# Optimization experiments

Measured on AMD Instinct MI355X. Metric: run time of the kernel, lower is better.

Reference implementation:

```python
import jax, jax.numpy as jnp
import numpy as np
import math

H = 16          # n_head
N_EMBD = 1024
EPS = 1e-5      # torch LayerNorm default


def setup_inputs() -> dict:
    key = jax.random.key(0)
    ks = jax.random.split(key, 6)
    B, T, C = 2, 2048, 1024
    x = jax.random.normal(ks[0], (B, T, C), dtype=jnp.float32)
    s = 0.02  # GPT-2 style init scale keeps softmax logits sane
    Wq = jax.random.normal(ks[1], (C, N_EMBD), dtype=jnp.float32) * s
    Wk = jax.random.normal(ks[2], (C, N_EMBD), dtype=jnp.float32) * s
    Wv = jax.random.normal(ks[3], (C, N_EMBD), dtype=jnp.float32) * s
    Wo = jax.random.normal(ks[4], (N_EMBD, C), dtype=jnp.float32) * s
    return {
        "x": x,
        "Wq": Wq, "bq": jnp.zeros((N_EMBD,), jnp.float32),
        "Wk": Wk, "bk": jnp.zeros((N_EMBD,), jnp.float32),
        "Wv": Wv, "bv": jnp.zeros((N_EMBD,), jnp.float32),
        "Wo": Wo, "bo": jnp.zeros((C,), jnp.float32),
        "gamma": jnp.ones((C,), jnp.float32),
        "beta": jnp.zeros((C,), jnp.float32),
    }


def reference(x, Wq, bq, Wk, bk, Wv, bv, Wo, bo, gamma, beta):
    B, T, _ = x.shape
    Dh = N_EMBD // H
    # projections -> (B, H, T, Dh)
    def split_heads(y):
        return y.reshape(B, T, H, Dh).transpose(0, 2, 1, 3)
    q = split_heads(x @ Wq + bq)
    k = split_heads(x @ Wk + bk)
    v = split_heads(x @ Wv + bv)
    # naive causal attention: explicit (B,H,T,T) scores
    att = jnp.einsum("bhtd,bhsd->bhts", q, k) * (1.0 / math.sqrt(Dh))
    causal = jnp.tril(jnp.ones((T, T), dtype=bool))
    att = jnp.where(causal[None, None], att, -jnp.inf)
    att = jax.nn.softmax(att, axis=-1)
    o = jnp.einsum("bhts,bhsd->bhtd", att, v)
    o = o.transpose(0, 2, 1, 3).reshape(B, T, N_EMBD)
    y = o @ Wo + bo
    # LayerNorm (dropout is identity at p=0 / eval)
    mu = jnp.mean(y, axis=-1, keepdims=True)
    var = jnp.var(y, axis=-1, keepdims=True)
    return (y - mu) * jax.lax.rsqrt(var + EPS) * gamma + beta
```

## Files before the change

kernel.cpp:

```cpp
#include <hip/hip_runtime.h>
#include <stdint.h>
#include <stddef.h>

typedef __attribute__((ext_vector_type(8))) short short8;
typedef __attribute__((ext_vector_type(4))) float f32x4;
typedef __attribute__((ext_vector_type(16))) float f32x16;
typedef __attribute__((ext_vector_type(4))) unsigned short us4;
typedef __attribute__((ext_vector_type(4))) unsigned u32x4;

#define DEVI static __device__ __forceinline__

DEVI unsigned short f2bf(float f) {
  unsigned u = __builtin_bit_cast(unsigned, f);
  u += 0x7FFFu + ((u >> 16) & 1u);
  return (unsigned short)(u >> 16);
}

DEVI f32x4 mfma16(short8 a, short8 b, f32x4 c) {
  return __builtin_amdgcn_mfma_f32_16x16x32_bf16(a, b, c, 0, 0, 0);
}

DEVI f32x16 mfma32(short8 a, short8 b, f32x16 c) {
  return __builtin_amdgcn_mfma_f32_32x32x16_bf16(a, b, c, 0, 0, 0);
}

DEVI unsigned cvtpk(float lo, float hi) {
  unsigned r;
  asm("v_cvt_pk_bf16_f32 %0, %1, %2" : "=v"(r) : "v"(lo), "v"(hi));
  return r;
}

DEVI void plswap(unsigned& a, unsigned& b) {
  asm("v_permlane32_swap_b32 %0, %1" : "+v"(a), "+v"(b));
}

DEVI float ex2(float x) {
  float r;
  asm("v_exp_f32 %0, %1" : "=v"(r) : "v"(x));
  return r;
}

DEVI float mx3(float a, float b, float c) {
  float r;
  asm("v_max3_f32 %0, %1, %2, %3" : "=v"(r) : "v"(a), "v"(b), "v"(c));
  return r;
}

DEVI f32x16 zero16() {
  f32x16 z;
#pragma unroll
  for (int i = 0; i < 16; ++i) z[i] = 0.f;
  return z;
}

DEVI void glds16(const void* g, void* l) {
  __builtin_amdgcn_global_load_lds(
      (const __attribute__((address_space(1))) void*)g,
      (__attribute__((address_space(3))) void*)l, 16, 0, 0);
}

__global__ __launch_bounds__(256) void k_cvt_x(const float* __restrict__ x,
                                               unsigned short* __restrict__ xb) {
  size_t i = ((size_t)blockIdx.x * 256 + threadIdx.x) * 8;
  f32x4 a = *(const f32x4*)(x + i);
  f32x4 b = *(const f32x4*)(x + i + 4);
  short8 v;
#pragma unroll
  for (int j = 0; j < 4; ++j) {
    v[j] = (short)f2bf(a[j]);
    v[4 + j] = (short)f2bf(b[j]);
  }
  *(short8*)(xb + i) = v;
}

__global__ __launch_bounds__(256) void k_twT4(const float* __restrict__ W0,
                                              const float* __restrict__ W1,
                                              const float* __restrict__ W2,
                                              const float* __restrict__ W3,
                                              unsigned short* __restrict__ WT) {
  __shared__ float tile[64][65];
  const int z = blockIdx.z;
  const float* W = (z == 0) ? W0 : (z == 1) ? W1 : (z == 2) ? W2 : W3;
  unsigned short* out = WT + (size_t)z * 1024 * 1024;
  const int n0 = blockIdx.x * 64, k0 = blockIdx.y * 64;
  const int t = threadIdx.x, rr = t >> 4, cc = (t & 15) * 4;
#pragma unroll
  for (int i = 0; i < 4; ++i) {
    int row = i * 16 + rr;
    f32x4 v = *(const f32x4*)(W + (size_t)(k0 + row) * 1024 + n0 + cc);
#pragma unroll
    for (int j = 0; j < 4; ++j) tile[row][cc + j] = v[j];
  }
  __syncthreads();
#pragma unroll
  for (int i = 0; i < 4; ++i) {
    int nrow = i * 16 + rr;
    us4 u;
#pragma unroll
    for (int j = 0; j < 4; ++j) u[j] = f2bf(tile[cc + j][nrow]);
    *(us4*)(out + (size_t)(n0 + nrow) * 1024 + k0 + cc) = u;
  }
}

template <bool SWAP>
DEVI void gemm_core2(const unsigned short* __restrict__ A,
                     const unsigned short* __restrict__ Bt,
                     int mt, int nt, char* lds, f32x4 (&acc)[4][4]) {
  const int t = threadIdx.x;
  const int l = t & 63, c = l & 15, g = l >> 4;
  const int w = t >> 6, wr = w >> 1, wc = w & 1;
  const int srow = t >> 3;
  const int sxor = (((t & 7) ^ (srow & 7))) * 8;
  const unsigned short* Ab = A + (size_t)(mt * 128 + srow) * 1024 + sxor;
  const unsigned short* Bb = Bt + (size_t)(nt * 128 + srow) * 1024 + sxor;
  const int key = (c & 7);

  auto STAGE = [&](int kt, int buf) {
    char* lb = lds + buf * 32768;
#pragma unroll
    for (int i = 0; i < 4; ++i) {
      glds16(Ab + (size_t)i * 32 * 1024 + kt * 64, lb + i * 4096 + t * 16);
      glds16(Bb + (size_t)i * 32 * 1024 + kt * 64, lb + 16384 + i * 4096 + t * 16);
    }
  };

  STAGE(0, 0);
  asm volatile("s_waitcnt vmcnt(0)" ::: "memory");
  __builtin_amdgcn_s_barrier();
  asm volatile("" ::: "memory");
  for (int kt = 0; kt < 16; ++kt) {
    const int cur = kt & 1;
    if (kt < 15) STAGE(kt + 1, cur ^ 1);
    const char* lb = lds + cur * 32768;
#pragma unroll
    for (int ks = 0; ks < 2; ++ks) {
      short8 af[4], bfr[4];
#pragma unroll
      for (int m = 0; m < 4; ++m)
        af[m] = *(const short8*)(lb + (wr * 64 + m * 16 + c) * 128 +
                                 ((ks * 4 + g) ^ key) * 16);
#pragma unroll
      for (int n = 0; n < 4; ++n)
        bfr[n] = *(const short8*)(lb + 16384 + (wc * 64 + n * 16 + c) * 128 +
                                  ((ks * 4 + g) ^ key) * 16);
#pragma unroll
      for (int m = 0; m < 4; ++m)
#pragma unroll
        for (int n = 0; n < 4; ++n)
          acc[m][n] = SWAP ? mfma16(bfr[n], af[m], acc[m][n])
                           : mfma16(af[m], bfr[n], acc[m][n]);
    }
    asm volatile("s_waitcnt vmcnt(0)" ::: "memory");
    __builtin_amdgcn_s_barrier();
    asm volatile("" ::: "memory");
  }
}

__global__ __launch_bounds__(256) void k_gemm_qkv(
    const unsigned short* __restrict__ A,
    const unsigned short* __restrict__ Wf,
    const float* __restrict__ b0, const float* __restrict__ b1, const float* __restrict__ b2,
    unsigned short* __restrict__ O0, unsigned short* __restrict__ O1,
    unsigned short* __restrict__ O2) {
  __shared__ char lds[65536];
  const int mt = blockIdx.x, ntz = blockIdx.y;
  const int z = ntz >> 3, ntl = ntz & 7;
  const float* bias = (z == 0) ? b0 : (z == 1) ? b1 : b2;
  unsigned short* out = (z == 0) ? O0 : (z == 1) ? O1 : O2;
  f32x4 acc[4][4];
#pragma unroll
  for (int m = 0; m < 4; ++m)
#pragma unroll
    for (int n = 0; n < 4; ++n) acc[m][n] = (f32x4){0.f, 0.f, 0.f, 0.f};
  const int t = threadIdx.x, l = t & 63, c = l & 15, g = l >> 4;
  const int w = t >> 6, wr = w >> 1, wc = w & 1;
  if (z < 2) {
    gemm_core2<true>(A, Wf, mt, ntz, lds, acc);
    const float sc = (z == 0) ? 0.18033688011f : 1.0f;
#pragma unroll
    for (int n = 0; n < 4; ++n) {
      int colb = ntl * 128 + wc * 64 + n * 16 + 4 * g;
      f32x4 bv4 = *(const f32x4*)(bias + colb);
      int h = colb >> 6, d = colb & 63;
#pragma unroll
      for (int m = 0; m < 4; ++m) {
        int rowg = mt * 128 + wr * 64 + m * 16 + c;
        int b = rowg >> 11, tt = rowg & 2047;
        us4 u;
#pragma unroll
        for (int r = 0; r < 4; ++r) u[r] = f2bf((acc[m][n][r] + bv4[r]) * sc);
        *(us4*)(out + ((size_t)(b * 16 + h) * 2048 + tt) * 64 + d) = u;
      }
    }
  } else {
    gemm_core2<false>(A, Wf, mt, ntz, lds, acc);
#pragma unroll
    for (int n = 0; n < 4; ++n) {
      int colg = ntl * 128 + wc * 64 + n * 16 + c;
      float bvv = bias[colg];
      int h = colg >> 6, d = colg & 63;
#pragma unroll
      for (int m = 0; m < 4; ++m) {
        int rowg = mt * 128 + wr * 64 + m * 16 + 4 * g;
        int b = rowg >> 11, tt = rowg & 2047;
        us4 u;
#pragma unroll
        for (int r = 0; r < 4; ++r) u[r] = f2bf(acc[m][n][r] + bvv);
        *(us4*)(out + ((size_t)(b * 16 + h) * 64 + d) * 2048 + tt) = u;
      }
    }
  }
}

__global__ __launch_bounds__(256) void k_gemm_proj(const unsigned short* __restrict__ A,
                                                   const unsigned short* __restrict__ Bt,
                                                   const float* __restrict__ bias,
                                                   float* __restrict__ Y) {
  __shared__ char lds[65536];
  f32x4 acc[4][4];
#pragma unroll
  for (int m = 0; m < 4; ++m)
#pragma unroll
    for (int n = 0; n < 4; ++n) acc[m][n] = (f32x4){0.f, 0.f, 0.f, 0.f};
  const int mt = blockIdx.x, nt = blockIdx.y;
  gemm_core2<true>(A, Bt, mt, nt, lds, acc);
  const int t = threadIdx.x, l = t & 63, c = l & 15, g = l >> 4;
  const int w = t >> 6, wr = w >> 1, wc = w & 1;
#pragma unroll
  for (int n = 0; n < 4; ++n) {
    int colb = nt * 128 + wc * 64 + n * 16 + 4 * g;
    f32x4 bv4 = *(const f32x4*)(bias + colb);
#pragma unroll
    for (int m = 0; m < 4; ++m) {
      int rowg = mt * 128 + wr * 64 + m * 16 + c;
      f32x4 o;
#pragma unroll
      for (int r = 0; r < 4; ++r) o[r] = acc[m][n][r] + bv4[r];
      *(f32x4*)(Y + (size_t)rowg * 1024 + colb) = o;
    }
  }
}

__global__ __launch_bounds__(128) void k_attn4(const unsigned short* __restrict__ Q,
                                               const unsigned short* __restrict__ K,
                                               const unsigned short* __restrict__ VT,
                                               unsigned short* __restrict__ O) {
  __shared__ char lds[32768];
  const int bid = blockIdx.x;
  const int half = bid >> 9, j = bid & 511;
  const int qt = half ? (j >> 5) : (31 - (j >> 5));
  const int bh = j & 31;
  const int t = threadIdx.x;
  const int w = t >> 6, l = t & 63;
  const int lq = l & 31, hi = l >> 5;
  const int q0 = qt * 64 + w * 32;
  const size_t kbase = (size_t)bh * 2048 * 64;
  const size_t vbase = (size_t)bh * 64 * 2048;
  const int srow = t >> 3;
  const int sx = ((t & 7) ^ (srow & 7)) * 8;
  const int NT = qt + 1;

  short8 qf[4];
#pragma unroll
  for (int ds = 0; ds < 4; ++ds)
    qf[ds] = *(const short8*)(Q + kbase + (size_t)(q0 + lq) * 64 + 16 * ds + 8 * hi);

  auto STAGE = [&](int kt, int buf) {
    const unsigned short* Kt = K + kbase + (size_t)kt * 4096;
    const unsigned short* Vt = VT + vbase + kt * 64;
    char* lb = lds + buf * 16384;
#pragma unroll
    for (int i = 0; i < 4; ++i) {
      int row = i * 16 + srow;
      glds16(Kt + (size_t)row * 64 + sx, lb + i * 2048 + t * 16);
      glds16(Vt + (size_t)row * 2048 + sx, lb + 8192 + i * 2048 + t * 16);
    }
  };

  f32x16 oacc[2];
  oacc[0] = zero16();
  oacc[1] = zero16();
  float m_s = -1e30f, l_s = 0.f;
  const int rx = lq & 7;

  STAGE(0, 0);
  for (int kt = 0; kt < NT; ++kt) {
    asm volatile("s_waitcnt vmcnt(0)" ::: "memory");
    __builtin_amdgcn_s_barrier();
    asm volatile("" ::: "memory");
    if (kt + 1 < NT) STAGE(kt + 1, (kt + 1) & 1);
    const char* lb = lds + (kt & 1) * 16384;
    const int kv0 = kt * 64;
    short8 kf0[4], kf1[4];
#pragma unroll
    for (int ds = 0; ds < 4; ++ds) {
      int blk = ((ds * 2 + hi) ^ rx) * 16;
      kf0[ds] = *(const short8*)(lb + lq * 128 + blk);
      kf1[ds] = *(const short8*)(lb + (lq + 32) * 128 + blk);
    }
    f32x16 st0 = zero16(), st1 = zero16();
    __builtin_amdgcn_s_setprio(1);
#pragma unroll
    for (int ds = 0; ds < 4; ++ds) {
      st0 = mfma32(kf0[ds], qf[ds], st0);
      st1 = mfma32(kf1[ds], qf[ds], st1);
    }
    __builtin_amdgcn_s_setprio(0);
    short8 vf[2][4];
#pragma unroll
    for (int fd = 0; fd < 2; ++fd) {
      int d = fd * 32 + lq;
#pragma unroll
      for (int s = 0; s < 4; ++s)
        vf[fd][s] = *(const short8*)(lb + 8192 + d * 128 + (((s * 2 + hi) ^ rx) * 16));
    }
    if (kt == NT - 1) {
      const int qg = q0 + lq;
#pragma unroll
      for (int r = 0; r < 16; ++r) {
        int kr = kv0 + (r & 3) + 8 * (r >> 2) + 4 * hi;
        if (kr > qg) st0[r] = -1e30f;
        if (kr + 32 > qg) st1[r] = -1e30f;
      }
    }
    float a8[8];
#pragma unroll
    for (int r = 0; r < 8; ++r)
      a8[r] = fmaxf(mx3(st0[r], st0[r + 8], st1[r]), st1[r + 8]);
    float mxv = mx3(mx3(a8[0], a8[1], a8[2]), mx3(a8[3], a8[4], a8[5]),
                    fmaxf(a8[6], a8[7]));
    mxv = fmaxf(mxv, __shfl_xor(mxv, 32, 64));
    if (!__all(mxv - m_s <= 11.5413f)) {
      float mnew = fmaxf(m_s, mxv);
      float corr = ex2(m_s - mnew);
      m_s = mnew;
      l_s *= corr;
#pragma unroll
      for (int r = 0; r < 16; ++r) {
        oacc[0][r] *= corr;
        oacc[1][r] *= corr;
      }
    }
    unsigned Wp[2][4][2];
    float gs[8];
#pragma unroll
    for (int f = 0; f < 2; ++f)
#pragma unroll
      for (int m4 = 0; m4 < 4; ++m4) {
        float p0 = ex2((f ? st1 : st0)[4 * m4 + 0] - m_s);
        float p1 = ex2((f ? st1 : st0)[4 * m4 + 1] - m_s);
        float p2 = ex2((f ? st1 : st0)[4 * m4 + 2] - m_s);
        float p3 = ex2((f ? st1 : st0)[4 * m4 + 3] - m_s);
        gs[f * 4 + m4] = (p0 + p1) + (p2 + p3);
        Wp[f][m4][0] = cvtpk(p0, p1);
        Wp[f][m4][1] = cvtpk(p2, p3);
      }
    float ps = ((gs[0] + gs[1]) + (gs[2] + gs[3])) + ((gs[4] + gs[5]) + (gs[6] + gs[7]));
    ps += __shfl_xor(ps, 32, 64);
    l_s += ps;
    __builtin_amdgcn_s_setprio(1);
#pragma unroll
    for (int s = 0; s < 4; ++s) {
      const int f = s >> 1, s2 = s & 1;
      unsigned a0 = Wp[f][2 * s2][0], b0 = Wp[f][2 * s2 + 1][0];
      unsigned a1 = Wp[f][2 * s2][1], b1 = Wp[f][2 * s2 + 1][1];
      plswap(a0, b0);
      plswap(a1, b1);
      u32x4 pw = {a0, a1, b0, b1};
      short8 pf = __builtin_bit_cast(short8, pw);
      oacc[0] = mfma32(vf[0][s], pf, oacc[0]);
      oacc[1] = mfma32(vf[1][s], pf, oacc[1]);
    }
    __builtin_amdgcn_s_setprio(0);
  }
  const float inv = 1.0f / l_s;
  const int b = bh >> 4, h = bh & 15;
  unsigned short* orow = O + ((size_t)b * 2048 + q0 + lq) * 1024 + h * 64 + 4 * hi;
#pragma unroll
  for (int f = 0; f < 2; ++f)
#pragma unroll
    for (int m4 = 0; m4 < 4; ++m4) {
      us4 u;
#pragma unroll
      for (int rr = 0; rr < 4; ++rr) u[rr] = f2bf(oacc[f][4 * m4 + rr] * inv);
      *(us4*)(orow + f * 32 + m4 * 8) = u;
    }
}

__global__ __launch_bounds__(256) void k_ln(const float* __restrict__ Y,
                                            const float* __restrict__ gamma,
                                            const float* __restrict__ beta,
                                            float* __restrict__ out) {
  __shared__ float red[8];
  const int row = blockIdx.x, t = threadIdx.x, w = t >> 6, l = t & 63;
  const float* yr = Y + (size_t)row * 1024;
  f32x4 v = *(const f32x4*)(yr + t * 4);
  float s = v[0] + v[1] + v[2] + v[3];
  float ss = v[0] * v[0] + v[1] * v[1] + v[2] * v[2] + v[3] * v[3];
#pragma unroll
  for (int d = 1; d < 64; d <<= 1) {
    s += __shfl_xor(s, d, 64);
    ss += __shfl_xor(ss, d, 64);
  }
  if (l == 0) {
    red[w] = s;
    red[4 + w] = ss;
  }
  __syncthreads();
  s = red[0] + red[1] + red[2] + red[3];
  ss = red[4] + red[5] + red[6] + red[7];
  float mean = s * (1.f / 1024.f);
  float var = ss * (1.f / 1024.f) - mean * mean;
  float rstd = rsqrtf(var + 1e-5f);
  f32x4 gv = *(const f32x4*)(gamma + t * 4);
  f32x4 bv = *(const f32x4*)(beta + t * 4);
  f32x4 ov;
#pragma unroll
  for (int j = 0; j < 4; ++j) ov[j] = (v[j] - mean) * rstd * gv[j] + bv[j];
  *(f32x4*)(out + (size_t)row * 1024 + t * 4) = ov;
}

extern "C" void kernel_launch(void* const* d_in, const int* in_sizes, int n_in,
                              void* d_out, int out_size, void* d_ws, size_t ws_size,
                              hipStream_t stream) {
  (void)in_sizes; (void)n_in; (void)out_size; (void)ws_size;
  const float* x = (const float*)d_in[0];
  const float* Wq = (const float*)d_in[1];
  const float* bq = (const float*)d_in[2];
  const float* Wk = (const float*)d_in[3];
  const float* bk = (const float*)d_in[4];
  const float* Wv = (const float*)d_in[5];
  const float* bv = (const float*)d_in[6];
  const float* Wo = (const float*)d_in[7];
  const float* bo = (const float*)d_in[8];
  const float* gamma = (const float*)d_in[9];
  const float* beta = (const float*)d_in[10];
  char* ws = (char*)d_ws;
  const size_t MB = 1024 * 1024;
  unsigned short* xb = (unsigned short*)(ws);
  unsigned short* WT = (unsigned short*)(ws + 8 * MB);
  unsigned short* WoT = (unsigned short*)(ws + 14 * MB);
  unsigned short* Qb = (unsigned short*)(ws + 16 * MB);
  unsigned short* Kb = (unsigned short*)(ws + 24 * MB);
  unsigned short* VTb = (unsigned short*)(ws + 32 * MB);
  unsigned short* Ob = (unsigned short*)(ws + 40 * MB);
  float* Y = (float*)(ws + 16 * MB);

  k_cvt_x<<<2048, 256, 0, stream>>>(x, xb);
  k_twT4<<<dim3(16, 16, 4), 256, 0, stream>>>(Wq, Wk, Wv, Wo, WT);
  k_gemm_qkv<<<dim3(32, 24), 256, 0, stream>>>(xb, WT, bq, bk, bv, Qb, Kb, VTb);
  k_attn4<<<1024, 128, 0, stream>>>(Qb, Kb, VTb, Ob);
  k_gemm_proj<<<dim3(32, 8), 256, 0, stream>>>(Ob, WoT, bo, Y);
  k_ln<<<4096, 256, 0, stream>>>(Y, gamma, beta, (float*)d_out);
}
```

Measured before the change: 116.9 us.

## Split long causal query tiles across two KV halves and merge partials

Query tiles 16–31 are each split into two blocks: one covers KV tiles 0–15 without masking, the other covers the remaining tiles up to the diagonal. Each writes unnormalized bf16 partial outputs plus running max and sum to workspace. A new merge kernel combines the two partials using rescaled weights. This caps per-block work at 16 KV tiles, to improve load balance and shorten the tail. The cost is one extra launch, extra partial-output traffic, and some precision loss from rounding the unnormalized partials to bf16.

```diff
diff --git a/kernel.cpp b/kernel.cpp
--- a/kernel.cpp
+++ b/kernel.cpp
@@ -14,6 +14,10 @@
   unsigned u = __builtin_bit_cast(unsigned, f);
   u += 0x7FFFu + ((u >> 16) & 1u);
   return (unsigned short)(u >> 16);
+}
+
+DEVI float bf2f(unsigned short u) {
+  return __builtin_bit_cast(float, ((unsigned)u) << 16);
 }
 
 DEVI f32x4 mfma16(short8 a, short8 b, f32x4 c) {
@@ -241,15 +245,25 @@
   }
 }
 
-__global__ __launch_bounds__(128) void k_attn4(const unsigned short* __restrict__ Q,
+__global__ __launch_bounds__(128) void k_attn5(const unsigned short* __restrict__ Q,
                                                const unsigned short* __restrict__ K,
                                                const unsigned short* __restrict__ VT,
-                                               unsigned short* __restrict__ O) {
+                                               unsigned short* __restrict__ O,
+                                               unsigned short* __restrict__ P,
+                                               float* __restrict__ ML) {
   __shared__ char lds[32768];
   const int bid = blockIdx.x;
-  const int half = bid >> 9, j = bid & 511;
-  const int qt = half ? (j >> 5) : (31 - (j >> 5));
-  const int bh = j & 31;
+  int qt, c0, nt, mode, bh;
+  if (bid < 512) {
+    mode = 1; qt = 16 + (bid >> 5); c0 = 0; nt = 16; bh = bid & 31;
+  } else {
+    int rem = bid - 512;
+    int v = 16 - (rem >> 6);
+    int sub = rem & 63;
+    bh = sub & 31;
+    if (sub < 32) { mode = 0; qt = v - 1;  c0 = 0;  nt = v; }
+    else          { mode = 2; qt = v + 15; c0 = 16; nt = v; }
+  }
   const int t = threadIdx.x;
   const int w = t >> 6, l = t & 63;
   const int lq = l & 31, hi = l >> 5;
@@ -258,16 +272,15 @@
   const size_t vbase = (size_t)bh * 64 * 2048;
   const int srow = t >> 3;
   const int sx = ((t & 7) ^ (srow & 7)) * 8;
-  const int NT = qt + 1;
 
   short8 qf[4];
 #pragma unroll
   for (int ds = 0; ds < 4; ++ds)
     qf[ds] = *(const short8*)(Q + kbase + (size_t)(q0 + lq) * 64 + 16 * ds + 8 * hi);
 
-  auto STAGE = [&](int kt, int buf) {
-    const unsigned short* Kt = K + kbase + (size_t)kt * 4096;
-    const unsigned short* Vt = VT + vbase + kt * 64;
+  auto STAGE = [&](int ktg, int buf) {
+    const unsigned short* Kt = K + kbase + (size_t)ktg * 4096;
+    const unsigned short* Vt = VT + vbase + ktg * 64;
     char* lb = lds + buf * 16384;
 #pragma unroll
     for (int i = 0; i < 4; ++i) {
@@ -283,14 +296,14 @@
   float m_s = -1e30f, l_s = 0.f;
   const int rx = lq & 7;
 
-  STAGE(0, 0);
-  for (int kt = 0; kt < NT; ++kt) {
+  STAGE(c0, 0);
+  for (int kt = 0; kt < nt; ++kt) {
     asm volatile("s_waitcnt vmcnt(0)" ::: "memory");
     __builtin_amdgcn_s_barrier();
     asm volatile("" ::: "memory");
-    if (kt + 1 < NT) STAGE(kt + 1, (kt + 1) & 1);
+    if (kt + 1 < nt) STAGE(c0 + kt + 1, (kt + 1) & 1);
     const char* lb = lds + (kt & 1) * 16384;
-    const int kv0 = kt * 64;
+    const int kv0 = (c0 + kt) * 64;
     short8 kf0[4], kf1[4];
 #pragma unroll
     for (int ds = 0; ds < 4; ++ds) {
@@ -314,7 +327,7 @@
       for (int s = 0; s < 4; ++s)
         vf[fd][s] = *(const short8*)(lb + 8192 + d * 128 + (((s * 2 + hi) ^ rx) * 16));
     }
-    if (kt == NT - 1) {
+    if (mode != 1 && kt == nt - 1) {
       const int qg = q0 + lq;
 #pragma unroll
       for (int r = 0; r < 16; ++r) {
@@ -373,18 +386,67 @@
     }
     __builtin_amdgcn_s_setprio(0);
   }
-  const float inv = 1.0f / l_s;
-  const int b = bh >> 4, h = bh & 15;
-  unsigned short* orow = O + ((size_t)b * 2048 + q0 + lq) * 1024 + h * 64 + 4 * hi;
-#pragma unroll
-  for (int f = 0; f < 2; ++f)
-#pragma unroll
-    for (int m4 = 0; m4 < 4; ++m4) {
-      us4 u;
-#pragma unroll
-      for (int rr = 0; rr < 4; ++rr) u[rr] = f2bf(oacc[f][4 * m4 + rr] * inv);
-      *(us4*)(orow + f * 32 + m4 * 8) = u;
-    }
+  if (mode == 0) {
+    const float inv = 1.0f / l_s;
+    const int b = bh >> 4, h = bh & 15;
+    unsigned short* orow = O + ((size_t)b * 2048 + q0 + lq) * 1024 + h * 64 + 4 * hi;
+#pragma unroll
+    for (int f = 0; f < 2; ++f)
+#pragma unroll
+      for (int m4 = 0; m4 < 4; ++m4) {
+        us4 u;
+#pragma unroll
+        for (int rr = 0; rr < 4; ++rr) u[rr] = f2bf(oacc[f][4 * m4 + rr] * inv);
+        *(us4*)(orow + f * 32 + m4 * 8) = u;
+      }
+  } else {
+    const int pid = ((qt - 16) * 32 + bh) * 2 + (mode - 1);
+    unsigned short* prow = P + (size_t)pid * 4096 + (w * 32 + lq) * 64 + 4 * hi;
+#pragma unroll
+    for (int f = 0; f < 2; ++f)
+#pragma unroll
+      for (int m4 = 0; m4 < 4; ++m4) {
+        us4 u;
+#pragma unroll
+        for (int rr = 0; rr < 4; ++rr) u[rr] = f2bf(oacc[f][4 * m4 + rr]);
+        *(us4*)(prow + f * 32 + m4 * 8) = u;
+      }
+    if (hi == 0) {
+      ML[pid * 128 + w * 32 + lq] = m_s;
+      ML[pid * 128 + 64 + w * 32 + lq] = l_s;
+    }
+  }
+}
+
+__global__ __launch_bounds__(64) void k_merge(const unsigned short* __restrict__ P,
+                                              const float* __restrict__ ML,
+                                              unsigned short* __restrict__ O) {
+  const int blk = blockIdx.x;
+  const int qt = 16 + (blk >> 5), bh = blk & 31;
+  const int pidA = ((qt - 16) * 32 + bh) * 2, pidB = pidA + 1;
+  const int r = threadIdx.x;
+  float mA = ML[pidA * 128 + r], lA = ML[pidA * 128 + 64 + r];
+  float mB = ML[pidB * 128 + r], lB = ML[pidB * 128 + 64 + r];
+  float mM = fmaxf(mA, mB);
+  float wA = ex2(mA - mM), wB = ex2(mB - mM);
+  float inv = 1.f / (lA * wA + lB * wB);
+  wA *= inv;
+  wB *= inv;
+  const unsigned short* pa = P + (size_t)pidA * 4096 + r * 64;
+  const unsigned short* pb = P + (size_t)pidB * 4096 + r * 64;
+  const int b = bh >> 4, h = bh & 15, q = qt * 64 + r;
+  unsigned short* orow = O + ((size_t)b * 2048 + q) * 1024 + h * 64;
+#pragma unroll
+  for (int j = 0; j < 8; ++j) {
+    short8 a = *(const short8*)(pa + j * 8);
+    short8 c = *(const short8*)(pb + j * 8);
+    short8 o;
+#pragma unroll
+    for (int k = 0; k < 8; ++k)
+      o[k] = (short)f2bf(bf2f((unsigned short)a[k]) * wA +
+                         bf2f((unsigned short)c[k]) * wB);
+    *(short8*)(orow + j * 8) = o;
+  }
 }
 
 __global__ __launch_bounds__(256) void k_ln(const float* __restrict__ Y,
@@ -445,11 +507,14 @@
   unsigned short* VTb = (unsigned short*)(ws + 32 * MB);
   unsigned short* Ob = (unsigned short*)(ws + 40 * MB);
   float* Y = (float*)(ws + 16 * MB);
+  unsigned short* Pp = (unsigned short*)(ws);
+  float* MLp = (float*)(ws + 8 * MB);
 
   k_cvt_x<<<2048, 256, 0, stream>>>(x, xb);
   k_twT4<<<dim3(16, 16, 4), 256, 0, stream>>>(Wq, Wk, Wv, Wo, WT);
   k_gemm_qkv<<<dim3(32, 24), 256, 0, stream>>>(xb, WT, bq, bk, bv, Qb, Kb, VTb);
-  k_attn4<<<1024, 128, 0, stream>>>(Qb, Kb, VTb, Ob);
+  k_attn5<<<1536, 128, 0, stream>>>(Qb, Kb, VTb, Ob, Pp, MLp);
+  k_merge<<<512, 64, 0, stream>>>(Pp, MLp, Ob);
   k_gemm_proj<<<dim3(32, 8), 256, 0, stream>>>(Ob, WoT, bo, Y);
   k_ln<<<4096, 256, 0, stream>>>(Y, gamma, beta, (float*)d_out);
 }
```

Result: no change. 118.6 us (+1.4%).
